# Performance work log

Hardware: AMD Instinct MI355X
Metric: run time of the kernel (lower is better)

The kernel has to match this reference:

```python
import jax, jax.numpy as jnp
import numpy as np

L, B, N, D, H = 2, 4, 2048, 1024, 16
DH = D // H
HID = 4 * D
EPS = 1e-5


def setup_inputs() -> dict:
    key = jax.random.key(0)
    ks = jax.random.split(key, 8)
    s = 0.02
    return {
        "tokens": jax.random.normal(ks[0], (B, N, D), jnp.float32),
        "ln1_g": jnp.ones((L, D), jnp.float32),
        "ln1_b": jnp.zeros((L, D), jnp.float32),
        "qkv_w": jax.random.normal(ks[1], (L, 3 * D, D), jnp.float32) * s,
        "qkv_b": jnp.zeros((L, 3 * D), jnp.float32),
        "out_w": jax.random.normal(ks[2], (L, D, D), jnp.float32) * s,
        "out_b": jnp.zeros((L, D), jnp.float32),
        "ln2_g": jnp.ones((L, D), jnp.float32),
        "ln2_b": jnp.zeros((L, D), jnp.float32),
        "fc1_w": jax.random.normal(ks[3], (L, HID, D), jnp.float32) * s,
        "fc1_b": jnp.zeros((L, HID), jnp.float32),
        "fc2_w": jax.random.normal(ks[4], (L, D, HID), jnp.float32) * s,
        "fc2_b": jnp.zeros((L, D), jnp.float32),
    }


def _layernorm(x, g, b):
    mu = jnp.mean(x, axis=-1, keepdims=True)
    var = jnp.mean(jnp.square(x - mu), axis=-1, keepdims=True)
    return (x - mu) * jax.lax.rsqrt(var + EPS) * g + b


def _mha(x, qkv_w, qkv_b, out_w, out_b):
    # nn.MultiheadAttention self-attention, batch_first=True
    qkv = x @ qkv_w.T + qkv_b                        # [B,N,3D]
    q, k, v = jnp.split(qkv, 3, axis=-1)
    q = q.reshape(B, N, H, DH)
    k = k.reshape(B, N, H, DH)
    v = v.reshape(B, N, H, DH)
    scores = jnp.einsum("bqhd,bkhd->bhqk", q, k) / np.sqrt(DH).astype(np.float32)
    attn = jax.nn.softmax(scores, axis=-1)
    o = jnp.einsum("bhqk,bkhd->bqhd", attn, v).reshape(B, N, D)
    return o @ out_w.T + out_b


def reference(tokens, ln1_g, ln1_b, qkv_w, qkv_b, out_w, out_b,
              ln2_g, ln2_b, fc1_w, fc1_b, fc2_w, fc2_b):
    x = tokens
    for i in range(L):
        # NOTE: the original reassigns tokens = norm1(tokens) before residual,
        # so the residual is taken on the NORMED tokens (faithful to source).
        x = _layernorm(x, ln1_g[i], ln1_b[i])
        x = x + _mha(x, qkv_w[i], qkv_b[i], out_w[i], out_b[i])
        x = _layernorm(x, ln2_g[i], ln2_b[i])
        h = jax.nn.gelu(x @ fc1_w[i].T + fc1_b[i], approximate=False)
        x = x + (h @ fc2_w[i].T + fc2_b[i])
    return x  # proj_out / norm_out are Identity since out_dim == dim
```

## Files before the change

kernel.cpp:

```cpp
#include <hip/hip_runtime.h>
#include <cstdint>
#include <cstddef>

typedef unsigned short u16;
typedef __attribute__((ext_vector_type(8))) short bf16x8;
typedef __attribute__((ext_vector_type(8))) u16  u16x8;
typedef __attribute__((ext_vector_type(4))) u16  u16x4;
typedef __attribute__((ext_vector_type(4))) float f32x4;
typedef __attribute__((ext_vector_type(16))) float f32x16;
typedef __attribute__((ext_vector_type(4))) unsigned u32x4;

static __device__ __forceinline__ u16 f2bf(float f) {
  unsigned u = __builtin_bit_cast(unsigned, f);
  u += 0x7fffu + ((u >> 16) & 1u);
  return (u16)(u >> 16);
}
static __device__ __forceinline__ float bf2f(u16 h) {
  return __builtin_bit_cast(float, (unsigned)h << 16);
}
static __device__ __forceinline__ unsigned cvtpk_bf16(float a, float b) {
  unsigned r;
  asm("v_cvt_pk_bf16_f32 %0, %1, %2" : "=v"(r) : "v"(a), "v"(b));
  return r;
}

static __device__ __forceinline__ void gload16(u16* lds, const u16* g) {
  __builtin_amdgcn_global_load_lds(
      (__attribute__((address_space(1))) unsigned int*)(void*)(g),
      (__attribute__((address_space(3))) unsigned int*)(lds), 16, 0, 0);
}

__global__ __launch_bounds__(256) void cast_f32_bf16(
    const float* __restrict__ s, u16* __restrict__ d, int n4) {
  int i = blockIdx.x * 256 + threadIdx.x;
  if (i < n4) {
    float4 v = ((const float4*)s)[i];
    u16x4 o;
    o[0] = f2bf(v.x); o[1] = f2bf(v.y); o[2] = f2bf(v.z); o[3] = f2bf(v.w);
    ((u16x4*)d)[i] = o;
  }
}

__global__ __launch_bounds__(256) void ln_kernel(
    const float* __restrict__ in, const float* __restrict__ g,
    const float* __restrict__ bb, float* __restrict__ outf,
    u16* __restrict__ outb) {
  const int row = blockIdx.x;
  const int t = threadIdx.x;
  const float4 v = ((const float4*)(in + (size_t)row * 1024))[t];
  float s  = v.x + v.y + v.z + v.w;
  float sq = v.x * v.x + v.y * v.y + v.z * v.z + v.w * v.w;
#pragma unroll
  for (int off = 32; off > 0; off >>= 1) {
    s  += __shfl_down(s, off);
    sq += __shfl_down(sq, off);
  }
  __shared__ float red[8];
  const int w = t >> 6;
  if ((t & 63) == 0) { red[w] = s; red[4 + w] = sq; }
  __syncthreads();
  const float ts  = red[0] + red[1] + red[2] + red[3];
  const float tsq = red[4] + red[5] + red[6] + red[7];
  const float mu = ts * (1.0f / 1024.0f);
  const float rv = rsqrtf(tsq * (1.0f / 1024.0f) - mu * mu + 1e-5f);
  const float4 gv = ((const float4*)g)[t];
  const float4 bv = ((const float4*)bb)[t];
  float4 y;
  y.x = (v.x - mu) * rv * gv.x + bv.x;
  y.y = (v.y - mu) * rv * gv.y + bv.y;
  y.z = (v.z - mu) * rv * gv.z + bv.z;
  y.w = (v.w - mu) * rv * gv.w + bv.w;
  ((float4*)(outf + (size_t)row * 1024))[t] = y;
  u16x4 ob;
  ob[0] = f2bf(y.x); ob[1] = f2bf(y.y); ob[2] = f2bf(y.z); ob[3] = f2bf(y.w);
  *(u16x4*)(outb + (size_t)row * 1024 + t * 4) = ob;
}

#define BM 128
#define BN 128
#define BK 32

template <int MODE>
__global__ __launch_bounds__(256) void gemm_bt(
    const u16* __restrict__ A, const u16* __restrict__ W,
    const float* __restrict__ bias, const float* __restrict__ res,
    u16* __restrict__ outb, float* __restrict__ outf, int Nn, int K) {
  __shared__ u16 As[BM * BK];
  __shared__ u16 Bs[BN * BK];
  const int t  = threadIdx.x;
  const int w  = t >> 6;
  const int ln = t & 63;
  const int lr = ln & 15;
  const int lg = ln >> 4;
  const int bm = blockIdx.x * BM;
  const int bn = blockIdx.y * BN;
  const int wm = (w >> 1) * 64;
  const int wn = (w & 1) * 64;

  f32x4 acc[4][4] = {};

  const int sr = t >> 2;
  const int sk = (t & 3) * 8;
  const u16* gA = A + (size_t)(bm + sr) * K + sk;
  const u16* gB = W + (size_t)(bn + sr) * K + sk;
  const int ldsOff = w * 512;

  const int kSteps = K >> 5;
  for (int kt = 0; kt < kSteps; ++kt) {
    __syncthreads();
    const u16* ga = gA + kt * BK;
    const u16* gb = gB + kt * BK;
    gload16(As + ldsOff,        ga);
    gload16(As + ldsOff + 2048, ga + (size_t)64 * K);
    gload16(Bs + ldsOff,        gb);
    gload16(Bs + ldsOff + 2048, gb + (size_t)64 * K);
    __syncthreads();

    bf16x8 af[4], bfr[4];
#pragma unroll
    for (int mi = 0; mi < 4; ++mi)
      af[mi] = *(const bf16x8*)(As + (wm + mi * 16 + lr) * BK + lg * 8);
#pragma unroll
    for (int ni = 0; ni < 4; ++ni)
      bfr[ni] = *(const bf16x8*)(Bs + (wn + ni * 16 + lr) * BK + lg * 8);
#pragma unroll
    for (int mi = 0; mi < 4; ++mi)
#pragma unroll
      for (int ni = 0; ni < 4; ++ni)
        acc[mi][ni] = __builtin_amdgcn_mfma_f32_16x16x32_bf16(
            af[mi], bfr[ni], acc[mi][ni], 0, 0, 0);
  }

#pragma unroll
  for (int ni = 0; ni < 4; ++ni) {
    const int col = bn + wn + ni * 16 + lr;
    const float bv = bias[col];
#pragma unroll
    for (int mi = 0; mi < 4; ++mi) {
      const int row0 = bm + wm + mi * 16 + lg * 4;
#pragma unroll
      for (int r = 0; r < 4; ++r) {
        float v = acc[mi][ni][r] + bv;
        const size_t idx = (size_t)(row0 + r) * Nn + col;
        if (MODE == 1) v = 0.5f * v * (1.0f + erff(v * 0.70710678118654752f));
        if (MODE == 2) outf[idx] = res[idx] + v;
        else           outb[idx] = f2bf(v);
      }
    }
  }
}

__global__ __launch_bounds__(256, 3) void attn_kernel(
    const u16* __restrict__ qkv, u16* __restrict__ o) {
  __shared__ u16 Ks[2 * 64 * 64];
  __shared__ u16 Vt[2 * 64 * 64];
  const int t   = threadIdx.x;
  const int w   = t >> 6;
  const int l   = t & 63;
  const int q31 = l & 31;
  const int h   = l >> 5;
  const int Lid = blockIdx.x;
  const int v_id = (Lid & 7) * 128 + (Lid >> 3);
  const int bh = v_id >> 4;
  const int b  = bh >> 4;
  const int hd = bh & 15;
  const int qb = (v_id & 15) * 128;
  const size_t baseRow = (size_t)b * 2048;
  const int hcol = hd * 64;

  bf16x8 qf[4];
  {
    const u16* qp = qkv + (baseRow + qb + w * 32 + q31) * 3072 + hcol + h * 8;
#pragma unroll
    for (int f = 0; f < 4; ++f) {
      u16x8 raw = *(const u16x8*)(qp + f * 16);
      bf16x8 q;
#pragma unroll
      for (int i = 0; i < 8; ++i)
        q[i] = (short)f2bf(bf2f(raw[i]) * 0.125f);
      qf[f] = q;
    }
  }

  f32x16 oacc[2] = {};
  float mrun = -3.0e38f, lrun = 0.0f;

  const int skey = t >> 3;
  const int dK   = 8 * ((t & 7) ^ (skey & 7));
  const int sd0  = (t & 7) * 8;

  {
    gload16(Ks + w * 512,        qkv + (baseRow + skey) * 3072      + 1024 + hcol + dK);
    gload16(Ks + 2048 + w * 512, qkv + (baseRow + 32 + skey) * 3072 + 1024 + hcol + dK);
    u16x8 va = *(const u16x8*)(qkv + (baseRow + skey) * 3072      + 2048 + hcol + sd0);
    u16x8 vb = *(const u16x8*)(qkv + (baseRow + 32 + skey) * 3072 + 2048 + hcol + sd0);
    char* VtB = (char*)Vt;
#pragma unroll
    for (int j = 0; j < 8; ++j) {
      const int sw = (j ^ (t & 7)) << 4;
      *(u16*)(VtB + ((((sd0 + j) * 128 + skey * 2)        ) ^ sw)) = va[j];
      *(u16*)(VtB + ((((sd0 + j) * 128 + (32 + skey) * 2) ) ^ sw)) = vb[j];
    }
  }
  __syncthreads();

  for (int kt = 0; kt < 32; ++kt) {
    char* const KsB = (char*)Ks + (kt & 1) * 8192;
    char* const VtB = (char*)Vt + (kt & 1) * 8192;
    u16* const KsN  = Ks + ((kt & 1) ^ 1) * 4096;
    char* const VtN = (char*)Vt + ((kt & 1) ^ 1) * 8192;

    u16x8 vva, vvb;
    const bool pf = (kt < 31);
    if (pf) {
      const size_t krow = baseRow + (size_t)(kt + 1) * 64;
      gload16(KsN + w * 512,        qkv + (krow + skey) * 3072      + 1024 + hcol + dK);
      gload16(KsN + 2048 + w * 512, qkv + (krow + 32 + skey) * 3072 + 1024 + hcol + dK);
      vva = *(const u16x8*)(qkv + (krow + skey) * 3072      + 2048 + hcol + sd0);
      vvb = *(const u16x8*)(qkv + (krow + 32 + skey) * 3072 + 2048 + hcol + sd0);
    }

    f32x16 s0 = {}, s1 = {};
#pragma unroll
    for (int f = 0; f < 4; ++f) {
      const int d0b = (f * 16 + h * 8) * 2;
      {
        const int row = q31;
        bf16x8 ka = *(const bf16x8*)(KsB + ((row * 128 + d0b) ^ ((row & 7) << 4)));
        s0 = __builtin_amdgcn_mfma_f32_32x32x16_bf16(ka, qf[f], s0, 0, 0, 0);
      }
      {
        const int row = 32 + q31;
        bf16x8 ka = *(const bf16x8*)(KsB + ((row * 128 + d0b) ^ ((row & 7) << 4)));
        s1 = __builtin_amdgcn_mfma_f32_32x32x16_bf16(ka, qf[f], s1, 0, 0, 0);
      }
    }

    float tm[16];
#pragma unroll
    for (int r = 0; r < 16; ++r) tm[r] = fmaxf(s0[r], s1[r]);
#pragma unroll
    for (int st = 8; st >= 1; st >>= 1)
#pragma unroll
      for (int r = 0; r < st; ++r) tm[r] = fmaxf(tm[r], tm[r + st]);
    const float mx = fmaxf(tm[0], __shfl_xor(tm[0], 32));
    const float mn = fmaxf(mrun, mx);
    const float al = __expf(mrun - mn);
    mrun = mn;
#pragma unroll
    for (int r = 0; r < 16; ++r) {
      s0[r] = __expf(s0[r] - mn);
      s1[r] = __expf(s1[r] - mn);
    }
    float tsum[16];
#pragma unroll
    for (int r = 0; r < 16; ++r) tsum[r] = s0[r] + s1[r];
#pragma unroll
    for (int st = 8; st >= 1; st >>= 1)
#pragma unroll
      for (int r = 0; r < st; ++r) tsum[r] += tsum[r + st];
    const float psum = tsum[0] + __shfl_xor(tsum[0], 32);
    lrun = lrun * al + psum;
#pragma unroll
    for (int r = 0; r < 16; ++r) { oacc[0][r] *= al; oacc[1][r] *= al; }

#pragma unroll
    for (int kw = 0; kw < 4; ++kw) {
      const int w1 = kw & 1;
      const f32x16 sv = (kw < 2) ? s0 : s1;
      const unsigned L0 = cvtpk_bf16(sv[8 * w1 + 0], sv[8 * w1 + 1]);
      const unsigned L1 = cvtpk_bf16(sv[8 * w1 + 2], sv[8 * w1 + 3]);
      const unsigned H0 = cvtpk_bf16(sv[8 * w1 + 4], sv[8 * w1 + 5]);
      const unsigned H1 = cvtpk_bf16(sv[8 * w1 + 6], sv[8 * w1 + 7]);
      const unsigned X0 = h ? L0 : H0;
      const unsigned X1 = h ? L1 : H1;
      const unsigned R0 = (unsigned)__shfl_xor((int)X0, 32);
      const unsigned R1 = (unsigned)__shfl_xor((int)X1, 32);
      u32x4 pw;
      pw[0] = h ? R0 : L0;
      pw[1] = h ? R1 : L1;
      pw[2] = h ? H0 : R0;
      pw[3] = h ? H1 : R1;
      const bf16x8 pb = __builtin_bit_cast(bf16x8, pw);
      const int k0b = (kw * 16 + h * 8) * 2;
#pragma unroll
      for (int dt = 0; dt < 2; ++dt) {
        const int d = dt * 32 + q31;
        bf16x8 va = *(const bf16x8*)(
            VtB + ((d * 128 + k0b) ^ ((((d & 7) ^ ((d >> 3) & 7))) << 4)));
        oacc[dt] = __builtin_amdgcn_mfma_f32_32x32x16_bf16(va, pb, oacc[dt], 0, 0, 0);
      }
    }

    if (pf) {
#pragma unroll
      for (int j = 0; j < 8; ++j) {
        const int sw = (j ^ (t & 7)) << 4;
        *(u16*)(VtN + ((((sd0 + j) * 128 + skey * 2)        ) ^ sw)) = vva[j];
        *(u16*)(VtN + ((((sd0 + j) * 128 + (32 + skey) * 2) ) ^ sw)) = vvb[j];
      }
    }
    __syncthreads();
  }

  const float inv = 1.0f / lrun;
  const size_t orow = baseRow + qb + w * 32 + q31;
#pragma unroll
  for (int dt = 0; dt < 2; ++dt)
#pragma unroll
    for (int g = 0; g < 4; ++g) {
      u16x4 ov;
#pragma unroll
      for (int j = 0; j < 4; ++j) ov[j] = f2bf(oacc[dt][g * 4 + j] * inv);
      *(u16x4*)(o + orow * 1024 + hcol + dt * 32 + g * 8 + h * 4) = ov;
    }
}

extern "C" void kernel_launch(void* const* d_in, const int* in_sizes, int n_in,
                              void* d_out, int out_size, void* d_ws,
                              size_t ws_size, hipStream_t stream) {
  const float* tokens = (const float*)d_in[0];
  const float* ln1_g  = (const float*)d_in[1];
  const float* ln1_b  = (const float*)d_in[2];
  const float* qkv_w  = (const float*)d_in[3];
  const float* qkv_b  = (const float*)d_in[4];
  const float* out_w  = (const float*)d_in[5];
  const float* out_b  = (const float*)d_in[6];
  const float* ln2_g  = (const float*)d_in[7];
  const float* ln2_b  = (const float*)d_in[8];
  const float* fc1_w  = (const float*)d_in[9];
  const float* fc1_b  = (const float*)d_in[10];
  const float* fc2_w  = (const float*)d_in[11];
  const float* fc2_b  = (const float*)d_in[12];
  float* xf = (float*)d_out;

  char* ws = (char*)d_ws;
  size_t off = 0;
  auto take = [&](size_t bytes) {
    char* p = ws + off;
    off += (bytes + 255) & ~(size_t)255;
    return p;
  };
  u16* xn    = (u16*)take((size_t)8192 * 1024 * 2);
  u16* big   = (u16*)take((size_t)8192 * 4096 * 2);
  u16* attnb = (u16*)take((size_t)8192 * 1024 * 2);
  u16* qkvw  = (u16*)take((size_t)2 * 3072 * 1024 * 2);
  u16* outw  = (u16*)take((size_t)2 * 1024 * 1024 * 2);
  u16* fc1w  = (u16*)take((size_t)2 * 4096 * 1024 * 2);
  u16* fc2w  = (u16*)take((size_t)2 * 1024 * 4096 * 2);
  u16* qkvb16 = big;
  u16* hb     = big;

  cast_f32_bf16<<<6144, 256, 0, stream>>>(qkv_w, qkvw, 2 * 3072 * 1024 / 4);
  cast_f32_bf16<<<2048, 256, 0, stream>>>(out_w, outw, 2 * 1024 * 1024 / 4);
  cast_f32_bf16<<<8192, 256, 0, stream>>>(fc1_w, fc1w, 2 * 4096 * 1024 / 4);
  cast_f32_bf16<<<8192, 256, 0, stream>>>(fc2_w, fc2w, 2 * 1024 * 4096 / 4);

  for (int i = 0; i < 2; ++i) {
    ln_kernel<<<8192, 256, 0, stream>>>(i == 0 ? tokens : xf,
                                        ln1_g + i * 1024, ln1_b + i * 1024, xf, xn);
    gemm_bt<0><<<dim3(64, 24), 256, 0, stream>>>(
        xn, qkvw + (size_t)i * 3072 * 1024, qkv_b + i * 3072, nullptr,
        qkvb16, nullptr, 3072, 1024);
    attn_kernel<<<1024, 256, 0, stream>>>(qkvb16, attnb);
    gemm_bt<2><<<dim3(64, 8), 256, 0, stream>>>(
        attnb, outw + (size_t)i * 1024 * 1024, out_b + i * 1024, xf,
        nullptr, xf, 1024, 1024);
    ln_kernel<<<8192, 256, 0, stream>>>(xf, ln2_g + i * 1024, ln2_b + i * 1024,
                                        xf, xn);
    gemm_bt<1><<<dim3(64, 32), 256, 0, stream>>>(
        xn, fc1w + (size_t)i * 4096 * 1024, fc1_b + i * 4096, nullptr,
        hb, nullptr, 4096, 1024);
    gemm_bt<2><<<dim3(64, 8), 256, 0, stream>>>(
        hb, fc2w + (size_t)i * 1024 * 4096, fc2_b + i * 1024, xf,
        nullptr, xf, 1024, 4096);
  }
}
```

Baseline: 1.049 ms.

## Replace GEMM with 256-row tiles, 4-stage LDS pipeline, 32x32 MFMA, swizzle

Replaces the single-buffered 128x128 GEMM with a 512-thread kernel that uses 256xBNT tiles, a four-stage ring of LDS buffers filled by async global_load_lds, and vmcnt-based waits, so global loads overlap compute. It moves to 32x32x16 MFMA, XOR-swizzles LDS reads to avoid bank conflicts, raises MFMA priority with setprio, and remaps block IDs so neighbouring blocks share L2 data. In exchange it uses more LDS and registers per block, which limits occupancy, and the 128-wide variant only fills 256 blocks.

```diff
diff --git a/kernel.cpp b/kernel.cpp
--- a/kernel.cpp
+++ b/kernel.cpp
@@ -29,6 +29,8 @@
       (__attribute__((address_space(1))) unsigned int*)(void*)(g),
       (__attribute__((address_space(3))) unsigned int*)(lds), 16, 0, 0);
 }
+
+#define GWAIT(n) asm volatile("s_waitcnt vmcnt(" #n ")" ::: "memory")
 
 __global__ __launch_bounds__(256) void cast_f32_bf16(
     const float* __restrict__ s, u16* __restrict__ d, int n4) {
@@ -76,75 +78,111 @@
   *(u16x4*)(outb + (size_t)row * 1024 + t * 4) = ob;
 }
 
-#define BM 128
-#define BN 128
-#define BK 32
-
-template <int MODE>
-__global__ __launch_bounds__(256) void gemm_bt(
+template <int MODE, int BNT>
+__global__ __launch_bounds__(512, 2) void gemm256(
     const u16* __restrict__ A, const u16* __restrict__ W,
     const float* __restrict__ bias, const float* __restrict__ res,
     u16* __restrict__ outb, float* __restrict__ outf, int Nn, int K) {
-  __shared__ u16 As[BM * BK];
-  __shared__ u16 Bs[BN * BK];
-  const int t  = threadIdx.x;
-  const int w  = t >> 6;
-  const int ln = t & 63;
-  const int lr = ln & 15;
-  const int lg = ln >> 4;
-  const int bm = blockIdx.x * BM;
-  const int bn = blockIdx.y * BN;
-  const int wm = (w >> 1) * 64;
-  const int wn = (w & 1) * 64;
-
-  f32x4 acc[4][4] = {};
-
-  const int sr = t >> 2;
-  const int sk = (t & 3) * 8;
-  const u16* gA = A + (size_t)(bm + sr) * K + sk;
-  const u16* gB = W + (size_t)(bn + sr) * K + sk;
-  const int ldsOff = w * 512;
-
-  const int kSteps = K >> 5;
-  for (int kt = 0; kt < kSteps; ++kt) {
-    __syncthreads();
-    const u16* ga = gA + kt * BK;
-    const u16* gb = gB + kt * BK;
-    gload16(As + ldsOff,        ga);
-    gload16(As + ldsOff + 2048, ga + (size_t)64 * K);
-    gload16(Bs + ldsOff,        gb);
-    gload16(Bs + ldsOff + 2048, gb + (size_t)64 * K);
-    __syncthreads();
-
-    bf16x8 af[4], bfr[4];
-#pragma unroll
-    for (int mi = 0; mi < 4; ++mi)
-      af[mi] = *(const bf16x8*)(As + (wm + mi * 16 + lr) * BK + lg * 8);
-#pragma unroll
-    for (int ni = 0; ni < 4; ++ni)
-      bfr[ni] = *(const bf16x8*)(Bs + (wn + ni * 16 + lr) * BK + lg * 8);
-#pragma unroll
-    for (int mi = 0; mi < 4; ++mi)
-#pragma unroll
-      for (int ni = 0; ni < 4; ++ni)
-        acc[mi][ni] = __builtin_amdgcn_mfma_f32_16x16x32_bf16(
-            af[mi], bfr[ni], acc[mi][ni], 0, 0, 0);
-  }
-
-#pragma unroll
-  for (int ni = 0; ni < 4; ++ni) {
-    const int col = bn + wn + ni * 16 + lr;
+  constexpr int NJ = BNT / 128;
+  constexpr int WN = BNT / 4;
+  constexpr int TS = (256 + BNT) * 32;
+  __shared__ u16 lds[4 * TS];
+  const int t   = threadIdx.x;
+  const int w   = t >> 6;
+  const int wm  = w >> 2;
+  const int wn  = w & 3;
+  const int q31 = t & 31;
+  const int lh  = (t >> 5) & 1;
+
+  const int cpx = (int)gridDim.x >> 3;
+  const int v   = ((int)blockIdx.x & 7) * cpx + ((int)blockIdx.x >> 3);
+  const int bm  = (v & 31) * 256;
+  const int bn  = (v >> 5) * BNT;
+
+  const int t0 = t & 1, t1 = (t >> 1) & 1, t2 = (t >> 2) & 1, t3 = (t >> 3) & 1;
+  const int srow = ((t >> 4) << 2) | (t3 << 1) | (t2 ^ t3);
+  const int scg  = ((t1 ^ t2 ^ t3) << 1) | t0;
+
+  f32x16 acc[4][NJ] = {};
+
+  const u16* const srcA0 = A + (size_t)(bm + srow) * K + scg * 8;
+  const u16* const srcB0 = W + (size_t)(bn + srow) * K + scg * 8;
+
+  auto stage = [&](int kt) {
+    u16* dst = lds + (size_t)(kt & 3) * TS;
+    const u16* sA = srcA0 + kt * 32;
+    gload16(dst +        w * 512, sA);
+    gload16(dst + 4096 + w * 512, sA + (size_t)128 * K);
+    const u16* sB = srcB0 + kt * 32;
+    gload16(dst + 8192 + w * 512, sB);
+    if constexpr (BNT == 256)
+      gload16(dst + 12288 + w * 512, sB + (size_t)128 * K);
+  };
+
+  auto compute = [&](int kt) {
+    const char* tb = (const char*)(lds + (size_t)(kt & 3) * TS);
+    const int sw = (q31 & 3) << 5;
+    bf16x8 af[4][2], bfr[NJ][2];
+#pragma unroll
+    for (int ai = 0; ai < 4; ++ai)
+#pragma unroll
+      for (int kk = 0; kk < 2; ++kk) {
+        const int lb = (wm * 128 + ai * 32 + q31) * 64 + kk * 32 + lh * 16;
+        af[ai][kk] = *(const bf16x8*)(tb + (lb ^ sw));
+      }
+#pragma unroll
+    for (int nj = 0; nj < NJ; ++nj)
+#pragma unroll
+      for (int kk = 0; kk < 2; ++kk) {
+        const int nb = 16384 + (wn * WN + nj * 32 + q31) * 64 + kk * 32 + lh * 16;
+        bfr[nj][kk] = *(const bf16x8*)(tb + (nb ^ sw));
+      }
+    __builtin_amdgcn_s_setprio(1);
+#pragma unroll
+    for (int kk = 0; kk < 2; ++kk)
+#pragma unroll
+      for (int ai = 0; ai < 4; ++ai)
+#pragma unroll
+        for (int nj = 0; nj < NJ; ++nj)
+          acc[ai][nj] = __builtin_amdgcn_mfma_f32_32x32x16_bf16(
+              af[ai][kk], bfr[nj][kk], acc[ai][nj], 0, 0, 0);
+    __builtin_amdgcn_s_setprio(0);
+  };
+
+  const int T = K >> 5;
+  stage(0); stage(1); stage(2);
+  if constexpr (BNT == 256) GWAIT(8); else GWAIT(6);
+  __builtin_amdgcn_s_barrier();
+  int kt = 0;
+  for (; kt + 3 < T; ++kt) {
+    stage(kt + 3);
+    compute(kt);
+    if constexpr (BNT == 256) GWAIT(8); else GWAIT(6);
+    __builtin_amdgcn_s_barrier();
+  }
+  compute(kt);
+  if constexpr (BNT == 256) GWAIT(4); else GWAIT(3);
+  __builtin_amdgcn_s_barrier();
+  compute(kt + 1);
+  GWAIT(0);
+  __builtin_amdgcn_s_barrier();
+  compute(kt + 2);
+
+#pragma unroll
+  for (int nj = 0; nj < NJ; ++nj) {
+    const int col = bn + wn * WN + nj * 32 + q31;
     const float bv = bias[col];
 #pragma unroll
-    for (int mi = 0; mi < 4; ++mi) {
-      const int row0 = bm + wm + mi * 16 + lg * 4;
-#pragma unroll
-      for (int r = 0; r < 4; ++r) {
-        float v = acc[mi][ni][r] + bv;
-        const size_t idx = (size_t)(row0 + r) * Nn + col;
-        if (MODE == 1) v = 0.5f * v * (1.0f + erff(v * 0.70710678118654752f));
-        if (MODE == 2) outf[idx] = res[idx] + v;
-        else           outb[idx] = f2bf(v);
+    for (int ai = 0; ai < 4; ++ai) {
+      const int row0 = bm + wm * 128 + ai * 32 + 4 * lh;
+#pragma unroll
+      for (int r = 0; r < 16; ++r) {
+        const int row = row0 + (r & 3) + 8 * (r >> 2);
+        float vv = acc[ai][nj][r] + bv;
+        const size_t idx = (size_t)row * Nn + col;
+        if (MODE == 1) vv = 0.5f * vv * (1.0f + erff(vv * 0.70710678118654752f));
+        if (MODE == 2) outf[idx] = res[idx] + vv;
+        else           outb[idx] = f2bf(vv);
       }
     }
   }
@@ -359,19 +397,19 @@
   for (int i = 0; i < 2; ++i) {
     ln_kernel<<<8192, 256, 0, stream>>>(i == 0 ? tokens : xf,
                                         ln1_g + i * 1024, ln1_b + i * 1024, xf, xn);
-    gemm_bt<0><<<dim3(64, 24), 256, 0, stream>>>(
+    gemm256<0, 256><<<384, 512, 0, stream>>>(
         xn, qkvw + (size_t)i * 3072 * 1024, qkv_b + i * 3072, nullptr,
         qkvb16, nullptr, 3072, 1024);
     attn_kernel<<<1024, 256, 0, stream>>>(qkvb16, attnb);
-    gemm_bt<2><<<dim3(64, 8), 256, 0, stream>>>(
+    gemm256<2, 128><<<256, 512, 0, stream>>>(
         attnb, outw + (size_t)i * 1024 * 1024, out_b + i * 1024, xf,
         nullptr, xf, 1024, 1024);
     ln_kernel<<<8192, 256, 0, stream>>>(xf, ln2_g + i * 1024, ln2_b + i * 1024,
                                         xf, xn);
-    gemm_bt<1><<<dim3(64, 32), 256, 0, stream>>>(
+    gemm256<1, 256><<<512, 512, 0, stream>>>(
         xn, fc1w + (size_t)i * 4096 * 1024, fc1_b + i * 4096, nullptr,
         hb, nullptr, 4096, 1024);
-    gemm_bt<2><<<dim3(64, 8), 256, 0, stream>>>(
+    gemm256<2, 128><<<256, 512, 0, stream>>>(
         hb, fc2w + (size_t)i * 1024 * 4096, fc2_b + i * 1024, xf,
         nullptr, xf, 1024, 4096);
   }
```

Measured after the change: 1.106 ms. 5.4% more time.
